# Kernel optimization log

Measured on AMD Instinct MI355X. Metric: run time of the kernel, lower is better.

The kernel has to match this reference:

```python
import jax, jax.numpy as jnp
import numpy as np

EPS = 1e-3  # slope floor epsilon from the module

def setup_inputs() -> dict:
    key = jax.random.key(0)
    k_in, k_xp = jax.random.split(key)
    B, F, K = 131072, 512, 31          # batch, feature, num_knot
    S = K + 1                          # num_spline
    inputs = jax.random.normal(k_in, (B, F), dtype=jnp.float32)
    x_pos = jax.random.normal(k_xp, (F, K), dtype=jnp.float32)   # nn.Parameter(torch.randn)
    slope = jnp.ones((F, S), dtype=jnp.float32)                  # nn.Parameter(torch.ones)
    y_bias = jnp.zeros((F, 1), dtype=jnp.float32)                # nn.Parameter(torch.zeros)
    return {"inputs": inputs, "x_pos": x_pos, "slope": slope, "y_bias": y_bias}

def reference(inputs, x_pos, slope, y_bias):
    # inputs: [B, F]; x_pos: [F, K]; slope: [F, K+1]; y_bias: [F, 1]
    slope_c = jax.nn.softplus(slope) + EPS                 # [F, S]
    xs = jnp.sort(x_pos, axis=1)                           # [F, K] sorted knots
    delta_x = jnp.roll(xs, -1, axis=1) - xs                # [F, K]
    delta_y = delta_x * slope_c[:, 1:]                     # [F, K]
    tmp = jnp.concatenate([xs[:, :1] + y_bias, delta_y[:, :-1]], axis=1)  # [F, K]
    y_pos = jnp.cumsum(tmp, axis=1)                        # [F, K] knot y-values

    # torchutils.searchsorted: count of knots <= input  ->  searchsorted(side='right')
    idx = jax.vmap(lambda k, v: jnp.searchsorted(k, v, side="right"),
                   in_axes=(0, 1), out_axes=1)(xs, inputs)  # [B, F] in [0, K]
    x_idx = jnp.maximum(idx - 1, 0)                         # [B, F] knot index

    # per-feature gathers (gather along dim 1 in torch, indices transposed)
    slope_sel = jnp.take_along_axis(slope_c, idx.T, axis=1).T   # [B, F]
    x_sel = jnp.take_along_axis(xs, x_idx.T, axis=1).T          # [B, F]
    y_sel = jnp.take_along_axis(y_pos, x_idx.T, axis=1).T       # [B, F]

    outputs = y_sel + (inputs - x_sel) * slope_sel
    return (outputs, slope_sel)
```

## Files before the change

### kernel.cpp

```cpp
#include <hip/hip_runtime.h>
#include <math.h>

#define B_DIM 131072
#define F_DIM 512
#define K_DIM 31
#define S_DIM 32
#define EPSV  1e-3f

#define TF        128
#define THREADS   256
#define GRID_X    (F_DIM / TF)
#define GRID_Y    512
#define ROWS_PER_Y   (B_DIM / GRID_Y)
#define SEGS         (TF / 4)
#define ROWS_PER_PASS (THREADS / SEGS)
#define ITERS        (ROWS_PER_Y / ROWS_PER_PASS)

__global__ __launch_bounds__(256) void plas_setup_kernel(
    const float* __restrict__ x_pos,
    const float* __restrict__ slope,
    const float* __restrict__ y_bias,
    float*  __restrict__ g_xs,
    float2* __restrict__ g_line)
{
    __shared__ float v[8][K_DIM];
    __shared__ float xs_s[8][K_DIM];
    __shared__ float sc[8][S_DIM];
    __shared__ float yp[8][K_DIM];

    const int tid = threadIdx.x;
    const int fb  = tid >> 5;
    const int k   = tid & 31;
    const int f   = blockIdx.x * 8 + fb;

    {
        float s = slope[f * S_DIM + k];
        sc[fb][k] = fmaxf(s, 0.0f) + log1pf(expf(-fabsf(s))) + EPSV;
    }
    if (k < K_DIM) v[fb][k] = x_pos[f * K_DIM + k];
    __syncthreads();

    if (k < K_DIM) {
        float val = v[fb][k];
        int rank = 0;
        #pragma unroll
        for (int j = 0; j < K_DIM; ++j) {
            float o = v[fb][j];
            rank += (o < val) || (o == val && j < k);
        }
        xs_s[fb][rank] = val;
    }
    __syncthreads();

    if (k == 0) {
        float y = xs_s[fb][0] + y_bias[f];
        yp[fb][0] = y;
        #pragma unroll
        for (int m = 1; m < K_DIM; ++m) {
            y += (xs_s[fb][m] - xs_s[fb][m - 1]) * sc[fb][m];
            yp[fb][m] = y;
        }
    }
    __syncthreads();

    {
        int xk = (k > 0) ? (k - 1) : 0;
        float so = sc[fb][k];
        float2 lb;
        lb.x = so;
        lb.y = yp[fb][xk] - xs_s[fb][xk] * so;
        g_line[f * S_DIM + k] = lb;
        if (k < K_DIM) g_xs[f * K_DIM + k] = xs_s[fb][k];
    }
}

__global__ __launch_bounds__(THREADS) void plas_main_kernel(
    const float*  __restrict__ inp,
    const float*  __restrict__ g_xs,
    const float2* __restrict__ g_line,
    float* __restrict__ out,
    float* __restrict__ ssel)
{
    __shared__ float  lxs[TF * 32];
    __shared__ float2 lline[TF * 32];

    const int tid = threadIdx.x;
    const int f0  = blockIdx.x * TF;

    {
        const int fl_base = tid >> 5;
        const int kk      = tid & 31;
        #pragma unroll
        for (int pass = 0; pass < TF / 8; ++pass) {
            const int fl  = pass * 8 + fl_base;
            const int swz = (fl >> 2) & 31;
            lline[fl * 32 + (kk ^ swz)] = g_line[(size_t)(f0 + fl) * S_DIM + kk];
            if (kk < K_DIM)
                lxs[fl * 32 + (kk ^ swz)] = g_xs[(size_t)(f0 + fl) * K_DIM + kk];
        }
    }
    __syncthreads();

    const int t4   = tid & 31;
    const int trow = tid >> 5;
    const int fbse = t4 * 4;
    const int swz  = t4;

    const float*  xsb = &lxs[fbse * 32];
    const float2* lnb = &lline[fbse * 32];

    size_t b = (size_t)blockIdx.y * ROWS_PER_Y + trow;

    for (int it = 0; it < ITERS; ++it) {
        const size_t base = b * F_DIM + f0 + fbse;
        const float4 x4 = *reinterpret_cast<const float4*>(inp + base);
        const float xv[4] = {x4.x, x4.y, x4.z, x4.w};
        float ov[4], sv[4];

        #pragma unroll
        for (int j = 0; j < 4; ++j) {
            const float* xs = xsb + j * 32;
            const float x = xv[j];
            int idx;
            idx  = (xs[15 ^ swz]        <= x) ? 16 : 0;
            idx += (xs[(idx + 7) ^ swz] <= x) ? 8 : 0;
            idx += (xs[(idx + 3) ^ swz] <= x) ? 4 : 0;
            idx += (xs[(idx + 1) ^ swz] <= x) ? 2 : 0;
            idx += (xs[idx ^ swz]       <= x) ? 1 : 0;
            const float2 lb = lnb[j * 32 + (idx ^ swz)];
            sv[j] = lb.x;
            ov[j] = fmaf(x, lb.x, lb.y);
        }

        *reinterpret_cast<float4*>(out  + base) = make_float4(ov[0], ov[1], ov[2], ov[3]);
        *reinterpret_cast<float4*>(ssel + base) = make_float4(sv[0], sv[1], sv[2], sv[3]);
        b += ROWS_PER_PASS;
    }
}

extern "C" void kernel_launch(void* const* d_in, const int* in_sizes, int n_in,
                              void* d_out, int out_size, void* d_ws, size_t ws_size,
                              hipStream_t stream) {
    const float* inputs = (const float*)d_in[0];
    const float* x_pos  = (const float*)d_in[1];
    const float* slope  = (const float*)d_in[2];
    const float* y_bias = (const float*)d_in[3];

    float* out  = (float*)d_out;
    float* ssel = (float*)d_out + (size_t)B_DIM * F_DIM;

    float2* g_line = (float2*)d_ws;
    float*  g_xs   = (float*)d_ws + (size_t)F_DIM * S_DIM * 2;

    plas_setup_kernel<<<F_DIM / 8, 256, 0, stream>>>(x_pos, slope, y_bias, g_xs, g_line);

    dim3 grid(GRID_X, GRID_Y);
    plas_main_kernel<<<grid, THREADS, 0, stream>>>(inputs, g_xs, g_line, out, ssel);
}
```

Measured before the change: 818.8 us.

## Halve feature tile, prefetch next row, and use nontemporal loads and stores

Shrinks the per-block feature tile from 128 to 64, which halves LDS use and doubles the grid in x, and adjusts the swizzle and thread mapping to match. The main loop now prefetches the next row's input one iteration ahead (software pipelining) and uses nontemporal loads and stores for the streaming input and both outputs, to cut cache pollution and hide load latency. Each block's LDS table is now read by twice as many blocks overall, and each thread holds one extra vector register.

```diff
diff --git a/kernel.cpp b/kernel.cpp
--- a/kernel.cpp
+++ b/kernel.cpp
@@ -7,7 +7,7 @@
 #define S_DIM 32
 #define EPSV  1e-3f
 
-#define TF        128
+#define TF        64
 #define THREADS   256
 #define GRID_X    (F_DIM / TF)
 #define GRID_Y    512
@@ -15,6 +15,9 @@
 #define SEGS         (TF / 4)
 #define ROWS_PER_PASS (THREADS / SEGS)
 #define ITERS        (ROWS_PER_Y / ROWS_PER_PASS)
+
+typedef float f4 __attribute__((ext_vector_type(4)));
+typedef float f2 __attribute__((ext_vector_type(2)));
 
 __global__ __launch_bounds__(256) void plas_setup_kernel(
     const float* __restrict__ x_pos,
@@ -81,8 +84,8 @@
     float* __restrict__ out,
     float* __restrict__ ssel)
 {
-    __shared__ float  lxs[TF * 32];
-    __shared__ float2 lline[TF * 32];
+    __shared__ float lxs[TF * 32];
+    __shared__ f2    lline[TF * 32];
 
     const int tid = threadIdx.x;
     const int f0  = blockIdx.x * TF;
@@ -93,48 +96,54 @@
         #pragma unroll
         for (int pass = 0; pass < TF / 8; ++pass) {
             const int fl  = pass * 8 + fl_base;
-            const int swz = (fl >> 2) & 31;
-            lline[fl * 32 + (kk ^ swz)] = g_line[(size_t)(f0 + fl) * S_DIM + kk];
+            const int swz = (fl >> 2) & (SEGS - 1);
+            const float2 g = g_line[(size_t)(f0 + fl) * S_DIM + kk];
+            f2 gv; gv[0] = g.x; gv[1] = g.y;
+            lline[fl * 32 + (kk ^ swz)] = gv;
             if (kk < K_DIM)
                 lxs[fl * 32 + (kk ^ swz)] = g_xs[(size_t)(f0 + fl) * K_DIM + kk];
         }
     }
     __syncthreads();
 
-    const int t4   = tid & 31;
-    const int trow = tid >> 5;
+    const int t4   = tid & (SEGS - 1);
+    const int trow = tid >> 4;
     const int fbse = t4 * 4;
     const int swz  = t4;
 
-    const float*  xsb = &lxs[fbse * 32];
-    const float2* lnb = &lline[fbse * 32];
+    const float* xsb = &lxs[fbse * 32];
+    const f2*    lnb = &lline[fbse * 32];
 
-    size_t b = (size_t)blockIdx.y * ROWS_PER_Y + trow;
+    const size_t stride = (size_t)ROWS_PER_PASS * F_DIM;
+    size_t base = ((size_t)blockIdx.y * ROWS_PER_Y + trow) * F_DIM + f0 + fbse;
+
+    f4 x4 = __builtin_nontemporal_load((const f4*)(inp + base));
 
     for (int it = 0; it < ITERS; ++it) {
-        const size_t base = b * F_DIM + f0 + fbse;
-        const float4 x4 = *reinterpret_cast<const float4*>(inp + base);
-        const float xv[4] = {x4.x, x4.y, x4.z, x4.w};
-        float ov[4], sv[4];
+        f4 xn = x4;
+        if (it + 1 < ITERS)
+            xn = __builtin_nontemporal_load((const f4*)(inp + base + stride));
 
+        f4 o4, s4;
         #pragma unroll
         for (int j = 0; j < 4; ++j) {
             const float* xs = xsb + j * 32;
-            const float x = xv[j];
+            const float x = x4[j];
             int idx;
             idx  = (xs[15 ^ swz]        <= x) ? 16 : 0;
             idx += (xs[(idx + 7) ^ swz] <= x) ? 8 : 0;
             idx += (xs[(idx + 3) ^ swz] <= x) ? 4 : 0;
             idx += (xs[(idx + 1) ^ swz] <= x) ? 2 : 0;
             idx += (xs[idx ^ swz]       <= x) ? 1 : 0;
-            const float2 lb = lnb[j * 32 + (idx ^ swz)];
-            sv[j] = lb.x;
-            ov[j] = fmaf(x, lb.x, lb.y);
+            const f2 lb = lnb[j * 32 + (idx ^ swz)];
+            s4[j] = lb[0];
+            o4[j] = fmaf(x, lb[0], lb[1]);
         }
 
-        *reinterpret_cast<float4*>(out  + base) = make_float4(ov[0], ov[1], ov[2], ov[3]);
-        *reinterpret_cast<float4*>(ssel + base) = make_float4(sv[0], sv[1], sv[2], sv[3]);
-        b += ROWS_PER_PASS;
+        __builtin_nontemporal_store(o4, (f4*)(out  + base));
+        __builtin_nontemporal_store(s4, (f4*)(ssel + base));
+        base += stride;
+        x4 = xn;
     }
 }
 
```

Measured after the change: 718.0 us. -12.3%, faster.
